# Performance work log

Hardware: AMD Instinct MI355X
Metric: run time of the kernel (lower is better)

The kernel has to match this reference:

```python
import jax, jax.numpy as jnp
import numpy as np

D = 128  # d_pair
N = 512  # n_res
B = 1
EPS = 1e-5


def setup_inputs() -> dict:
    key = jax.random.key(0)
    ks = jax.random.split(key, 16)
    s = 0.02
    inp = {
        "pair": jax.random.normal(ks[0], (B, N, N, D), dtype=jnp.float32),
        "pair_mask": jnp.ones((B, N, N), dtype=jnp.float32),
        "ln_g": jnp.ones((D,), dtype=jnp.float32),
        "ln_b": jnp.zeros((D,), dtype=jnp.float32),
        "w_lp": jax.random.normal(ks[1], (D, D), dtype=jnp.float32) * s,
        "b_lp": jnp.zeros((D,), dtype=jnp.float32),
        "w_lg": jax.random.normal(ks[2], (D, D), dtype=jnp.float32) * s,
        "b_lg": jnp.zeros((D,), dtype=jnp.float32),
        "w_rp": jax.random.normal(ks[3], (D, D), dtype=jnp.float32) * s,
        "b_rp": jnp.zeros((D,), dtype=jnp.float32),
        "w_rg": jax.random.normal(ks[4], (D, D), dtype=jnp.float32) * s,
        "b_rg": jnp.zeros((D,), dtype=jnp.float32),
        "w_g": jax.random.normal(ks[5], (D, D), dtype=jnp.float32) * s,
        "b_g": jnp.zeros((D,), dtype=jnp.float32),
        "w_o": jax.random.normal(ks[6], (D, D), dtype=jnp.float32) * s,
        "b_o": jnp.zeros((D,), dtype=jnp.float32),
    }
    return inp


def _layer_norm(x, g, b):
    mu = jnp.mean(x, axis=-1, keepdims=True)
    var = jnp.mean(jnp.square(x - mu), axis=-1, keepdims=True)
    return (x - mu) * jax.lax.rsqrt(var + EPS) * g + b


def reference(pair, pair_mask, ln_g, ln_b, w_lp, b_lp, w_lg, b_lg,
              w_rp, b_rp, w_rg, b_rg, w_g, b_g, w_o, b_o):
    # [B,N,N,D] pair representation; outgoing triangle multiplication
    x = _layer_norm(pair, ln_g, ln_b)
    mask = pair_mask[..., None]  # [B,N,N,1]
    left = (x @ w_lp + b_lp) * jax.nn.sigmoid(x @ w_lg + b_lg) * mask
    right = (x @ w_rp + b_rp) * jax.nn.sigmoid(x @ w_rg + b_rg) * mask
    # outgoing: contract over j -> per-channel NxN matmul
    out = jnp.einsum('bijd,bjkd->bikd', left, right)
    out = out * jax.nn.sigmoid(x @ w_g + b_g)
    out = out @ w_o + b_o
    return out
```

## Files before the change

kernel.cpp:

```cpp
#include <hip/hip_runtime.h>

#define NN 512
#define DD 128
#define PP (NN*NN)

typedef __attribute__((ext_vector_type(8))) short short8;
typedef __attribute__((ext_vector_type(4))) short shortx4;
typedef __attribute__((ext_vector_type(4))) float floatx4;

__device__ __forceinline__ unsigned short f2bf(float f) {
  unsigned int u = __float_as_uint(f);
  u += 0x7fffu + ((u >> 16) & 1u);
  return (unsigned short)(u >> 16);
}
__device__ __forceinline__ float bf2f(unsigned short h) {
  return __uint_as_float(((unsigned int)h) << 16);
}
__device__ __forceinline__ float sigm(float x) {
  return 1.f / (1.f + __expf(-x));
}

__device__ __forceinline__ void gload_lds16(const unsigned short* g, unsigned short* l) {
  __builtin_amdgcn_global_load_lds(
      (const __attribute__((address_space(1))) unsigned int*)g,
      (__attribute__((address_space(3))) unsigned int*)l, 16, 0, 0);
}

__global__ void k0_prep(const float* __restrict__ wlp, const float* __restrict__ wlg,
                        const float* __restrict__ wrp, const float* __restrict__ wrg,
                        const float* __restrict__ wg,  const float* __restrict__ wo,
                        unsigned short* __restrict__ wt) {
  const float* src[6] = {wlp, wlg, wrp, wrg, wg, wo};
  int m = blockIdx.y;
  int idx = blockIdx.x * 256 + threadIdx.x;
  int d = idx >> 7, e = idx & 127;
  wt[m * 16384 + e * 128 + d] = f2bf(src[m][d * 128 + e]);
}

__device__ __forceinline__ void run_mm(const unsigned short* __restrict__ wt_m,
                                       unsigned short* Alds, unsigned short* Wlds,
                                       int t, int wm, int we, int ln, int q8,
                                       floatx4 (&acc)[4][4]) {
  #pragma unroll
  for (int it = 0; it < 8; ++it) {
    int flat = it * 256 + t;
    int e = flat >> 4, c = flat & 15;
    *(short8*)&Wlds[e * 136 + c * 8] = *(const short8*)(wt_m + e * 128 + c * 8);
  }
  __syncthreads();
  #pragma unroll
  for (int ks = 0; ks < 4; ++ks) {
    short8 a[4], b[4];
    #pragma unroll
    for (int i = 0; i < 4; ++i)
      a[i] = *(const short8*)&Alds[(wm + i * 16 + ln) * 136 + ks * 32 + q8 * 8];
    #pragma unroll
    for (int i = 0; i < 4; ++i)
      b[i] = *(const short8*)&Wlds[(we + i * 16 + ln) * 136 + ks * 32 + q8 * 8];
    #pragma unroll
    for (int i = 0; i < 4; ++i)
      #pragma unroll
      for (int j = 0; j < 4; ++j)
        acc[i][j] = __builtin_amdgcn_mfma_f32_16x16x32_bf16(a[i], b[j], acc[i][j], 0, 0, 0);
  }
  __syncthreads();
}

__launch_bounds__(256, 2)
__global__ void k1_ln_proj(const float* __restrict__ pair, const float* __restrict__ pmask,
                           const float* __restrict__ lng, const float* __restrict__ lnb,
                           const unsigned short* __restrict__ wt,
                           const float* __restrict__ b_lp, const float* __restrict__ b_lg,
                           const float* __restrict__ b_rp, const float* __restrict__ b_rg,
                           const float* __restrict__ b_g,
                           unsigned short* __restrict__ left_t,
                           unsigned short* __restrict__ right_bt,
                           unsigned short* __restrict__ gate_t) {
  __shared__ __align__(16) unsigned short Alds[128 * 136];
  __shared__ __align__(16) unsigned short Wlds[128 * 136];
  __shared__ float Mlds[128];

  const int t = threadIdx.x;
  const int unit = blockIdx.y;
  const int q = blockIdx.x;

  long prow0, pstride, mrow0, mstride, soff;
  if (unit == 1) {
    int j0 = (q >> 9) << 7, k0 = q & 511;
    prow0 = ((long)j0 * NN + k0) * DD; pstride = (long)NN * DD;
    mrow0 = (long)j0 * NN + k0;        mstride = NN;
    soff  = (long)k0 * NN + j0;
  } else {
    long p0 = (long)q << 7;
    prow0 = p0 * DD; pstride = DD;
    mrow0 = p0;      mstride = 1;
    soff  = p0;
  }

  {
    int r = t >> 1, h = t & 1;
    const float* row = pair + prow0 + (long)r * pstride + h * 64;
    floatx4 v[16];
    float s = 0.f, s2 = 0.f;
    #pragma unroll
    for (int c = 0; c < 16; ++c) {
      v[c] = *(const floatx4*)(row + c * 4);
      s  += v[c].x + v[c].y + v[c].z + v[c].w;
      s2 += v[c].x * v[c].x + v[c].y * v[c].y + v[c].z * v[c].z + v[c].w * v[c].w;
    }
    s  += __shfl_xor(s, 1);
    s2 += __shfl_xor(s2, 1);
    float mu = s * (1.f / 128.f);
    float var = s2 * (1.f / 128.f) - mu * mu;
    float rs = rsqrtf(var + 1e-5f);
    #pragma unroll
    for (int c = 0; c < 16; ++c) {
      floatx4 g4 = *(const floatx4*)(lng + h * 64 + c * 4);
      floatx4 b4 = *(const floatx4*)(lnb + h * 64 + c * 4);
      shortx4 pk;
      pk[0] = (short)f2bf((v[c].x - mu) * rs * g4.x + b4.x);
      pk[1] = (short)f2bf((v[c].y - mu) * rs * g4.y + b4.y);
      pk[2] = (short)f2bf((v[c].z - mu) * rs * g4.z + b4.z);
      pk[3] = (short)f2bf((v[c].w - mu) * rs * g4.w + b4.w);
      *(shortx4*)&Alds[r * 136 + h * 64 + c * 4] = pk;
    }
    if (h == 0) Mlds[r] = pmask[mrow0 + (long)r * mstride];
  }
  __syncthreads();

  const int lane = t & 63, w = t >> 6;
  const int ln = lane & 15, q8 = lane >> 4;
  const int wm = (w >> 1) << 6, we = (w & 1) << 6;

  unsigned short* stg = (w < 2) ? (Alds + w * 4608) : (Wlds + (w - 2) * 4608);

  if (unit < 2) {
    floatx4 accA[4][4] = {};
    floatx4 accB[4][4] = {};
    run_mm(wt + (unit == 0 ? 0 : 2) * 16384, Alds, Wlds, t, wm, we, ln, q8, accA);
    run_mm(wt + (unit == 0 ? 1 : 3) * 16384, Alds, Wlds, t, wm, we, ln, q8, accB);
    const float* bpp = (unit == 0) ? b_lp : b_rp;
    const float* bgg = (unit == 0) ? b_lg : b_rg;
    #pragma unroll
    for (int j = 0; j < 4; ++j) {
      int eg = we + j * 16 + ln;
      float bp_v = bpp[eg], bg_v = bgg[eg];
      #pragma unroll
      for (int i = 0; i < 4; ++i) {
        shortx4 pk;
        #pragma unroll
        for (int r = 0; r < 4; ++r) {
          int m = wm + i * 16 + q8 * 4 + r;
          float val = (accA[i][j][r] + bp_v) * sigm(accB[i][j][r] + bg_v) * Mlds[m];
          pk[r] = (short)f2bf(val);
        }
        *(shortx4*)&stg[(j * 16 + ln) * 72 + i * 16 + q8 * 4] = pk;
      }
    }
  } else {
    floatx4 accA[4][4] = {};
    run_mm(wt + 4 * 16384, Alds, Wlds, t, wm, we, ln, q8, accA);
    #pragma unroll
    for (int j = 0; j < 4; ++j) {
      int eg = we + j * 16 + ln;
      float bg_v = b_g[eg];
      #pragma unroll
      for (int i = 0; i < 4; ++i) {
        shortx4 pk;
        #pragma unroll
        for (int r = 0; r < 4; ++r)
          pk[r] = (short)f2bf(sigm(accA[i][j][r] + bg_v));
        *(shortx4*)&stg[(j * 16 + ln) * 72 + i * 16 + q8 * 4] = pk;
      }
    }
  }
  __syncthreads();

  unsigned short* dstbase = (unit == 0) ? left_t : (unit == 1 ? right_bt : gate_t);
  #pragma unroll
  for (int itr = 0; itr < 8; ++itr) {
    int row = itr * 8 + (lane >> 3);
    int c = lane & 7;
    short8 vv = *(const short8*)&stg[row * 72 + c * 8];
    long eg = we + row;
    *(short8*)(dstbase + eg * PP + soff + wm + c * 8) = vv;
  }
}

__launch_bounds__(256, 3)
__global__ void k2_einsum(const unsigned short* __restrict__ left_t,
                          const unsigned short* __restrict__ right_bt,
                          const unsigned short* __restrict__ gate_t,
                          unsigned short* __restrict__ tmpg) {
  __shared__ __align__(16) unsigned short Al[128 * 32];
  __shared__ __align__(16) unsigned short Bl[128 * 32];
  const int t = threadIdx.x;
  const int d = blockIdx.y;
  const int i0 = (blockIdx.x >> 2) << 7;
  const int k0 = (blockIdx.x & 3) << 7;
  const unsigned short* Ag = left_t   + (long)d * PP;
  const unsigned short* Bg = right_bt + (long)d * PP;
  const int lane = t & 63, w = t >> 6;
  const int ln = lane & 15, q8 = lane >> 4;
  const int wm = (w >> 1) << 6, wn = (w & 1) << 6;

  floatx4 acc[4][4] = {};
  for (int j0 = 0; j0 < NN; j0 += 32) {
    #pragma unroll
    for (int it = 0; it < 2; ++it) {
      int flat = it * 256 + t;
      int r = flat >> 2, c = flat & 3;
      gload_lds16(Ag + (long)(i0 + r) * NN + j0 + c * 8, &Al[flat * 8]);
    }
    #pragma unroll
    for (int it = 0; it < 2; ++it) {
      int flat = it * 256 + t;
      int r = flat >> 2, c = flat & 3;
      gload_lds16(Bg + (long)(k0 + r) * NN + j0 + c * 8, &Bl[flat * 8]);
    }
    __syncthreads();
    short8 a[4], b[4];
    #pragma unroll
    for (int i = 0; i < 4; ++i)
      a[i] = *(const short8*)&Al[(wm + i * 16 + ln) * 32 + q8 * 8];
    #pragma unroll
    for (int i = 0; i < 4; ++i)
      b[i] = *(const short8*)&Bl[(wn + i * 16 + ln) * 32 + q8 * 8];
    #pragma unroll
    for (int i = 0; i < 4; ++i)
      #pragma unroll
      for (int j = 0; j < 4; ++j)
        acc[i][j] = __builtin_amdgcn_mfma_f32_16x16x32_bf16(a[i], b[j], acc[i][j], 0, 0, 0);
    __syncthreads();
  }
  const unsigned short* Gg = gate_t + (long)d * PP;
  unsigned short* Og = tmpg + (long)d * PP;
  #pragma unroll
  for (int i = 0; i < 4; ++i)
    #pragma unroll
    for (int j = 0; j < 4; ++j) {
      int n = k0 + wn + j * 16 + ln;
      #pragma unroll
      for (int r = 0; r < 4; ++r) {
        int m = i0 + wm + i * 16 + q8 * 4 + r;
        long idx = (long)m * NN + n;
        Og[idx] = f2bf(acc[i][j][r] * bf2f(Gg[idx]));
      }
    }
}

__launch_bounds__(256, 2)
__global__ void k3_out(const unsigned short* __restrict__ tmpg,
                       const unsigned short* __restrict__ wt,
                       const float* __restrict__ b_o,
                       float* __restrict__ out) {
  __shared__ __align__(16) unsigned short Tl[128 * 136];
  __shared__ __align__(16) unsigned short Wl[128 * 136];
  const int t = threadIdx.x;
  const long p0 = (long)blockIdx.x << 7;
  const unsigned short* wo = wt + 5 * 16384;

  #pragma unroll
  for (int it = 0; it < 8; ++it) {
    int flat = it * 256 + t;
    int e = flat >> 4, c = flat & 15;
    *(short8*)&Wl[e * 136 + c * 8] = *(const short8*)(wo + e * 128 + c * 8);
  }
  #pragma unroll
  for (int it = 0; it < 8; ++it) {
    int flat = it * 256 + t;
    int dd2 = flat >> 4, c = flat & 15;
    *(short8*)&Tl[dd2 * 136 + c * 8] = *(const short8*)(tmpg + (long)dd2 * PP + p0 + c * 8);
  }
  __syncthreads();

  const int lane = t & 63, w = t >> 6;
  const int ln = lane & 15, q8 = lane >> 4;
  const int wm = (w >> 1) << 6, wn = (w & 1) << 6;

  floatx4 acc[4][4] = {};
  #pragma unroll
  for (int ks = 0; ks < 4; ++ks) {
    short8 a[4], b[4];
    #pragma unroll
    for (int i = 0; i < 4; ++i) {
      int m = wm + i * 16 + ln;
      short8 av;
      #pragma unroll
      for (int jj = 0; jj < 8; ++jj)
        av[jj] = (short)Tl[(ks * 32 + q8 * 8 + jj) * 136 + m];
      a[i] = av;
    }
    #pragma unroll
    for (int i = 0; i < 4; ++i)
      b[i] = *(const short8*)&Wl[(wn + i * 16 + ln) * 136 + ks * 32 + q8 * 8];
    #pragma unroll
    for (int i = 0; i < 4; ++i)
      #pragma unroll
      for (int j = 0; j < 4; ++j)
        acc[i][j] = __builtin_amdgcn_mfma_f32_16x16x32_bf16(a[i], b[j], acc[i][j], 0, 0, 0);
  }
  #pragma unroll
  for (int j = 0; j < 4; ++j) {
    int eg = wn + j * 16 + ln;
    float bias = b_o[eg];
    #pragma unroll
    for (int i = 0; i < 4; ++i)
      #pragma unroll
      for (int r = 0; r < 4; ++r) {
        int m = wm + i * 16 + q8 * 4 + r;
        out[(p0 + m) * DD + eg] = acc[i][j][r] + bias;
      }
  }
}

extern "C" void kernel_launch(void* const* d_in, const int* in_sizes, int n_in,
                              void* d_out, int out_size, void* d_ws, size_t ws_size,
                              hipStream_t stream) {
  const float* pair = (const float*)d_in[0];
  const float* pmask = (const float*)d_in[1];
  const float* ln_g = (const float*)d_in[2];
  const float* ln_b = (const float*)d_in[3];
  const float* w_lp = (const float*)d_in[4];
  const float* b_lp = (const float*)d_in[5];
  const float* w_lg = (const float*)d_in[6];
  const float* b_lg = (const float*)d_in[7];
  const float* w_rp = (const float*)d_in[8];
  const float* b_rp = (const float*)d_in[9];
  const float* w_rg = (const float*)d_in[10];
  const float* b_rg = (const float*)d_in[11];
  const float* w_g  = (const float*)d_in[12];
  const float* b_g  = (const float*)d_in[13];
  const float* w_o  = (const float*)d_in[14];
  const float* b_o  = (const float*)d_in[15];
  float* out = (float*)d_out;

  char* ws = (char*)d_ws;
  unsigned short* wt       = (unsigned short*)ws;
  unsigned short* left_t   = (unsigned short*)(ws + 196608);
  unsigned short* right_bt = left_t   + (size_t)PP * DD;
  unsigned short* gate_t   = right_bt + (size_t)PP * DD;
  unsigned short* tmpg     = gate_t   + (size_t)PP * DD;

  k0_prep<<<dim3(64, 6), 256, 0, stream>>>(w_lp, w_lg, w_rp, w_rg, w_g, w_o, wt);
  k1_ln_proj<<<dim3(2048, 3), 256, 0, stream>>>(pair, pmask, ln_g, ln_b, wt,
      b_lp, b_lg, b_rp, b_rg, b_g, left_t, right_bt, gate_t);
  k2_einsum<<<dim3(16, 128), 256, 0, stream>>>(left_t, right_bt, gate_t, tmpg);
  k3_out<<<dim3(2048), 256, 0, stream>>>(tmpg, wt, b_o, out);
}
```

Before: 527.9 us.

## Split layernorm into own kernel, stream projection K-chunks, move gating into output kernel

LayerNorm now runs once in a separate kernel that writes bf16 normalized activations, so the three projection units no longer recompute it from fp32 pair. The projection kernel streams 32-wide K chunks through LDS with direct global-to-LDS loads and fuses the projection and gate matmuls into one loop. The einsum kernel stages its output through LDS so it can write coalesced 16-byte stores without reading the gate. The gate multiply moves into the output kernel, which builds a transposed A tile in LDS and reads W_o straight from global memory. Packed bf16 conversion instructions are also added. The cost is an extra xln buffer round-trip through memory and an extra kernel launch.

```diff
diff --git a/kernel.cpp b/kernel.cpp
--- a/kernel.cpp
+++ b/kernel.cpp
@@ -7,6 +7,7 @@
 typedef __attribute__((ext_vector_type(8))) short short8;
 typedef __attribute__((ext_vector_type(4))) short shortx4;
 typedef __attribute__((ext_vector_type(4))) float floatx4;
+typedef __attribute__((ext_vector_type(4))) unsigned int uintx4;
 
 __device__ __forceinline__ unsigned short f2bf(float f) {
   unsigned int u = __float_as_uint(f);
@@ -15,6 +16,11 @@
 }
 __device__ __forceinline__ float bf2f(unsigned short h) {
   return __uint_as_float(((unsigned int)h) << 16);
+}
+__device__ __forceinline__ unsigned int pkbf2(float lo, float hi) {
+  unsigned int r;
+  asm("v_cvt_pk_bf16_f32 %0, %1, %2" : "=v"(r) : "v"(lo), "v"(hi));
+  return r;
 }
 __device__ __forceinline__ float sigm(float x) {
   return 1.f / (1.f + __expf(-x));
@@ -37,151 +43,166 @@
   wt[m * 16384 + e * 128 + d] = f2bf(src[m][d * 128 + e]);
 }
 
-__device__ __forceinline__ void run_mm(const unsigned short* __restrict__ wt_m,
-                                       unsigned short* Alds, unsigned short* Wlds,
-                                       int t, int wm, int we, int ln, int q8,
-                                       floatx4 (&acc)[4][4]) {
-  #pragma unroll
-  for (int it = 0; it < 8; ++it) {
-    int flat = it * 256 + t;
-    int e = flat >> 4, c = flat & 15;
-    *(short8*)&Wlds[e * 136 + c * 8] = *(const short8*)(wt_m + e * 128 + c * 8);
-  }
-  __syncthreads();
-  #pragma unroll
-  for (int ks = 0; ks < 4; ++ks) {
-    short8 a[4], b[4];
-    #pragma unroll
-    for (int i = 0; i < 4; ++i)
-      a[i] = *(const short8*)&Alds[(wm + i * 16 + ln) * 136 + ks * 32 + q8 * 8];
-    #pragma unroll
-    for (int i = 0; i < 4; ++i)
-      b[i] = *(const short8*)&Wlds[(we + i * 16 + ln) * 136 + ks * 32 + q8 * 8];
-    #pragma unroll
-    for (int i = 0; i < 4; ++i)
-      #pragma unroll
-      for (int j = 0; j < 4; ++j)
-        acc[i][j] = __builtin_amdgcn_mfma_f32_16x16x32_bf16(a[i], b[j], acc[i][j], 0, 0, 0);
-  }
-  __syncthreads();
+__launch_bounds__(256, 4)
+__global__ void k1a_ln(const float* __restrict__ pair,
+                       const float* __restrict__ lng, const float* __restrict__ lnb,
+                       unsigned short* __restrict__ xln) {
+  const int t = threadIdx.x;
+  const long p0 = (long)blockIdx.x << 7;
+  const int r = t >> 1, h = t & 1;
+  const float* row = pair + (p0 + r) * DD + h * 64;
+  floatx4 v[16];
+  float s = 0.f, s2 = 0.f;
+  #pragma unroll
+  for (int c = 0; c < 16; ++c) {
+    v[c] = *(const floatx4*)(row + c * 4);
+    s  += v[c].x + v[c].y + v[c].z + v[c].w;
+    s2 += v[c].x * v[c].x + v[c].y * v[c].y + v[c].z * v[c].z + v[c].w * v[c].w;
+  }
+  s  += __shfl_xor(s, 1);
+  s2 += __shfl_xor(s2, 1);
+  float mu = s * (1.f / 128.f);
+  float var = s2 * (1.f / 128.f) - mu * mu;
+  float rs = rsqrtf(var + 1e-5f);
+  unsigned short* orow = xln + (p0 + r) * DD + h * 64;
+  #pragma unroll
+  for (int c2 = 0; c2 < 8; ++c2) {
+    floatx4 g0 = *(const floatx4*)(lng + h * 64 + c2 * 8);
+    floatx4 g1 = *(const floatx4*)(lng + h * 64 + c2 * 8 + 4);
+    floatx4 b0 = *(const floatx4*)(lnb + h * 64 + c2 * 8);
+    floatx4 b1 = *(const floatx4*)(lnb + h * 64 + c2 * 8 + 4);
+    floatx4 a = v[2 * c2], b = v[2 * c2 + 1];
+    uintx4 u;
+    u[0] = pkbf2((a.x - mu) * rs * g0.x + b0.x, (a.y - mu) * rs * g0.y + b0.y);
+    u[1] = pkbf2((a.z - mu) * rs * g0.z + b0.z, (a.w - mu) * rs * g0.w + b0.w);
+    u[2] = pkbf2((b.x - mu) * rs * g1.x + b1.x, (b.y - mu) * rs * g1.y + b1.y);
+    u[3] = pkbf2((b.z - mu) * rs * g1.z + b1.z, (b.w - mu) * rs * g1.w + b1.w);
+    *(uintx4*)(orow + c2 * 8) = u;
+  }
 }
 
 __launch_bounds__(256, 2)
-__global__ void k1_ln_proj(const float* __restrict__ pair, const float* __restrict__ pmask,
-                           const float* __restrict__ lng, const float* __restrict__ lnb,
-                           const unsigned short* __restrict__ wt,
-                           const float* __restrict__ b_lp, const float* __restrict__ b_lg,
-                           const float* __restrict__ b_rp, const float* __restrict__ b_rg,
-                           const float* __restrict__ b_g,
-                           unsigned short* __restrict__ left_t,
-                           unsigned short* __restrict__ right_bt,
-                           unsigned short* __restrict__ gate_t) {
-  __shared__ __align__(16) unsigned short Alds[128 * 136];
-  __shared__ __align__(16) unsigned short Wlds[128 * 136];
+__global__ void k1b_proj(const unsigned short* __restrict__ xln,
+                         const float* __restrict__ pmask,
+                         const unsigned short* __restrict__ wt,
+                         const float* __restrict__ b_lp, const float* __restrict__ b_lg,
+                         const float* __restrict__ b_rp, const float* __restrict__ b_rg,
+                         const float* __restrict__ b_g,
+                         unsigned short* __restrict__ left_t,
+                         unsigned short* __restrict__ right_bt,
+                         unsigned short* __restrict__ gate_t) {
+  __shared__ __align__(16) unsigned short Sm[17408];
   __shared__ float Mlds[128];
+  unsigned short* Al = Sm;
+  unsigned short* Bp = Sm + 4096;
+  unsigned short* Bg = Sm + 8192;
 
   const int t = threadIdx.x;
   const int unit = blockIdx.y;
   const int q = blockIdx.x;
 
-  long prow0, pstride, mrow0, mstride, soff;
+  int j0 = 0, kk = 0;
+  long p0 = 0, soff;
   if (unit == 1) {
-    int j0 = (q >> 9) << 7, k0 = q & 511;
-    prow0 = ((long)j0 * NN + k0) * DD; pstride = (long)NN * DD;
-    mrow0 = (long)j0 * NN + k0;        mstride = NN;
-    soff  = (long)k0 * NN + j0;
+    j0 = (q >> 9) << 7; kk = q & 511;
+    soff = (long)kk * NN + j0;
   } else {
-    long p0 = (long)q << 7;
-    prow0 = p0 * DD; pstride = DD;
-    mrow0 = p0;      mstride = 1;
-    soff  = p0;
-  }
-
-  {
-    int r = t >> 1, h = t & 1;
-    const float* row = pair + prow0 + (long)r * pstride + h * 64;
-    floatx4 v[16];
-    float s = 0.f, s2 = 0.f;
-    #pragma unroll
-    for (int c = 0; c < 16; ++c) {
-      v[c] = *(const floatx4*)(row + c * 4);
-      s  += v[c].x + v[c].y + v[c].z + v[c].w;
-      s2 += v[c].x * v[c].x + v[c].y * v[c].y + v[c].z * v[c].z + v[c].w * v[c].w;
-    }
-    s  += __shfl_xor(s, 1);
-    s2 += __shfl_xor(s2, 1);
-    float mu = s * (1.f / 128.f);
-    float var = s2 * (1.f / 128.f) - mu * mu;
-    float rs = rsqrtf(var + 1e-5f);
-    #pragma unroll
-    for (int c = 0; c < 16; ++c) {
-      floatx4 g4 = *(const floatx4*)(lng + h * 64 + c * 4);
-      floatx4 b4 = *(const floatx4*)(lnb + h * 64 + c * 4);
-      shortx4 pk;
-      pk[0] = (short)f2bf((v[c].x - mu) * rs * g4.x + b4.x);
-      pk[1] = (short)f2bf((v[c].y - mu) * rs * g4.y + b4.y);
-      pk[2] = (short)f2bf((v[c].z - mu) * rs * g4.z + b4.z);
-      pk[3] = (short)f2bf((v[c].w - mu) * rs * g4.w + b4.w);
-      *(shortx4*)&Alds[r * 136 + h * 64 + c * 4] = pk;
-    }
-    if (h == 0) Mlds[r] = pmask[mrow0 + (long)r * mstride];
-  }
-  __syncthreads();
+    p0 = (long)q << 7;
+    soff = p0;
+  }
+  auto arow = [&](int r) -> long {
+    return (unit == 1) ? ((long)(j0 + r) * NN + kk) : (p0 + r);
+  };
+
+  if (unit < 2 && t < 128) Mlds[t] = pmask[arow(t)];
+
+  const unsigned short* wA = wt + (unit == 0 ? 0 : unit == 1 ? 2 : 4) * 16384;
+  const unsigned short* wB = wt + (unit == 0 ? 1 : 3) * 16384;
 
   const int lane = t & 63, w = t >> 6;
   const int ln = lane & 15, q8 = lane >> 4;
   const int wm = (w >> 1) << 6, we = (w & 1) << 6;
-
-  unsigned short* stg = (w < 2) ? (Alds + w * 4608) : (Wlds + (w - 2) * 4608);
-
+  const int sr = t >> 2, sc = t & 3;
+
+  floatx4 aP[4][4] = {}, aG[4][4] = {};
+  for (int kc = 0; kc < 4; ++kc) {
+    gload_lds16(xln + arow(sr) * DD + kc * 32 + sc * 8,      &Al[t * 8]);
+    gload_lds16(xln + arow(sr + 64) * DD + kc * 32 + sc * 8, &Al[(256 + t) * 8]);
+    gload_lds16(wA + sr * 128 + kc * 32 + sc * 8,            &Bp[t * 8]);
+    gload_lds16(wA + (sr + 64) * 128 + kc * 32 + sc * 8,     &Bp[(256 + t) * 8]);
+    if (unit < 2) {
+      gload_lds16(wB + sr * 128 + kc * 32 + sc * 8,          &Bg[t * 8]);
+      gload_lds16(wB + (sr + 64) * 128 + kc * 32 + sc * 8,   &Bg[(256 + t) * 8]);
+    }
+    __syncthreads();
+    short8 a[4];
+    #pragma unroll
+    for (int i = 0; i < 4; ++i)
+      a[i] = *(const short8*)&Al[(wm + i * 16 + ln) * 32 + q8 * 8];
+    #pragma unroll
+    for (int j = 0; j < 4; ++j) {
+      short8 bpv = *(const short8*)&Bp[(we + j * 16 + ln) * 32 + q8 * 8];
+      #pragma unroll
+      for (int i = 0; i < 4; ++i)
+        aP[i][j] = __builtin_amdgcn_mfma_f32_16x16x32_bf16(a[i], bpv, aP[i][j], 0, 0, 0);
+    }
+    if (unit < 2) {
+      #pragma unroll
+      for (int j = 0; j < 4; ++j) {
+        short8 bgv = *(const short8*)&Bg[(we + j * 16 + ln) * 32 + q8 * 8];
+        #pragma unroll
+        for (int i = 0; i < 4; ++i)
+          aG[i][j] = __builtin_amdgcn_mfma_f32_16x16x32_bf16(a[i], bgv, aG[i][j], 0, 0, 0);
+      }
+    }
+    __syncthreads();
+  }
+
+  unsigned short* mystg = Sm + w * 4352;
   if (unit < 2) {
-    floatx4 accA[4][4] = {};
-    floatx4 accB[4][4] = {};
-    run_mm(wt + (unit == 0 ? 0 : 2) * 16384, Alds, Wlds, t, wm, we, ln, q8, accA);
-    run_mm(wt + (unit == 0 ? 1 : 3) * 16384, Alds, Wlds, t, wm, we, ln, q8, accB);
     const float* bpp = (unit == 0) ? b_lp : b_rp;
     const float* bgg = (unit == 0) ? b_lg : b_rg;
     #pragma unroll
     for (int j = 0; j < 4; ++j) {
       int eg = we + j * 16 + ln;
-      float bp_v = bpp[eg], bg_v = bgg[eg];
+      float bp = bpp[eg], bg = bgg[eg];
       #pragma unroll
       for (int i = 0; i < 4; ++i) {
-        shortx4 pk;
+        float vv[4];
         #pragma unroll
         for (int r = 0; r < 4; ++r) {
           int m = wm + i * 16 + q8 * 4 + r;
-          float val = (accA[i][j][r] + bp_v) * sigm(accB[i][j][r] + bg_v) * Mlds[m];
-          pk[r] = (short)f2bf(val);
+          vv[r] = (aP[i][j][r] + bp) * sigm(aG[i][j][r] + bg) * Mlds[m];
         }
-        *(shortx4*)&stg[(j * 16 + ln) * 72 + i * 16 + q8 * 4] = pk;
+        unsigned int* du = (unsigned int*)&mystg[(j * 16 + ln) * 68 + i * 16 + q8 * 4];
+        du[0] = pkbf2(vv[0], vv[1]);
+        du[1] = pkbf2(vv[2], vv[3]);
       }
     }
   } else {
-    floatx4 accA[4][4] = {};
-    run_mm(wt + 4 * 16384, Alds, Wlds, t, wm, we, ln, q8, accA);
     #pragma unroll
     for (int j = 0; j < 4; ++j) {
       int eg = we + j * 16 + ln;
-      float bg_v = b_g[eg];
+      float bg = b_g[eg];
       #pragma unroll
       for (int i = 0; i < 4; ++i) {
-        shortx4 pk;
+        float vv[4];
         #pragma unroll
         for (int r = 0; r < 4; ++r)
-          pk[r] = (short)f2bf(sigm(accA[i][j][r] + bg_v));
-        *(shortx4*)&stg[(j * 16 + ln) * 72 + i * 16 + q8 * 4] = pk;
+          vv[r] = sigm(aP[i][j][r] + bg);
+        unsigned int* du = (unsigned int*)&mystg[(j * 16 + ln) * 68 + i * 16 + q8 * 4];
+        du[0] = pkbf2(vv[0], vv[1]);
+        du[1] = pkbf2(vv[2], vv[3]);
       }
     }
   }
-  __syncthreads();
 
   unsigned short* dstbase = (unit == 0) ? left_t : (unit == 1 ? right_bt : gate_t);
   #pragma unroll
   for (int itr = 0; itr < 8; ++itr) {
     int row = itr * 8 + (lane >> 3);
     int c = lane & 7;
-    short8 vv = *(const short8*)&stg[row * 72 + c * 8];
+    short8 vv = *(const short8*)&mystg[row * 68 + c * 8];
     long eg = we + row;
     *(short8*)(dstbase + eg * PP + soff + wm + c * 8) = vv;
   }
@@ -190,10 +211,11 @@
 __launch_bounds__(256, 3)
 __global__ void k2_einsum(const unsigned short* __restrict__ left_t,
                           const unsigned short* __restrict__ right_bt,
-                          const unsigned short* __restrict__ gate_t,
                           unsigned short* __restrict__ tmpg) {
-  __shared__ __align__(16) unsigned short Al[128 * 32];
-  __shared__ __align__(16) unsigned short Bl[128 * 32];
+  __shared__ __align__(16) unsigned short Sm[128 * 132];
+  unsigned short* Al = Sm;
+  unsigned short* Bl = Sm + 128 * 32;
+  unsigned short* Cl = Sm;
   const int t = threadIdx.x;
   const int d = blockIdx.y;
   const int i0 = (blockIdx.x >> 2) << 7;
@@ -233,44 +255,58 @@
         acc[i][j] = __builtin_amdgcn_mfma_f32_16x16x32_bf16(a[i], b[j], acc[i][j], 0, 0, 0);
     __syncthreads();
   }
-  const unsigned short* Gg = gate_t + (long)d * PP;
+  #pragma unroll
+  for (int i = 0; i < 4; ++i)
+    #pragma unroll
+    for (int j = 0; j < 4; ++j) {
+      int n = wn + j * 16 + ln;
+      #pragma unroll
+      for (int r = 0; r < 4; ++r)
+        Cl[(wm + i * 16 + q8 * 4 + r) * 132 + n] = f2bf(acc[i][j][r]);
+    }
+  __syncthreads();
   unsigned short* Og = tmpg + (long)d * PP;
   #pragma unroll
-  for (int i = 0; i < 4; ++i)
-    #pragma unroll
-    for (int j = 0; j < 4; ++j) {
-      int n = k0 + wn + j * 16 + ln;
-      #pragma unroll
-      for (int r = 0; r < 4; ++r) {
-        int m = i0 + wm + i * 16 + q8 * 4 + r;
-        long idx = (long)m * NN + n;
-        Og[idx] = f2bf(acc[i][j][r] * bf2f(Gg[idx]));
-      }
-    }
-}
-
-__launch_bounds__(256, 2)
+  for (int it = 0; it < 8; ++it) {
+    int flat = it * 256 + t;
+    int m = flat >> 4, c = flat & 15;
+    *(short8*)(Og + (long)(i0 + m) * NN + k0 + c * 8) = *(const short8*)&Cl[m * 132 + c * 8];
+  }
+}
+
+__launch_bounds__(256, 3)
 __global__ void k3_out(const unsigned short* __restrict__ tmpg,
+                       const unsigned short* __restrict__ gate_t,
                        const unsigned short* __restrict__ wt,
                        const float* __restrict__ b_o,
                        float* __restrict__ out) {
-  __shared__ __align__(16) unsigned short Tl[128 * 136];
-  __shared__ __align__(16) unsigned short Wl[128 * 136];
+  __shared__ __align__(16) unsigned short Tl[128 * 144];
+  unsigned int* TlU = (unsigned int*)Tl;
   const int t = threadIdx.x;
   const long p0 = (long)blockIdx.x << 7;
   const unsigned short* wo = wt + 5 * 16384;
 
   #pragma unroll
-  for (int it = 0; it < 8; ++it) {
+  for (int it = 0; it < 4; ++it) {
     int flat = it * 256 + t;
-    int e = flat >> 4, c = flat & 15;
-    *(short8*)&Wl[e * 136 + c * 8] = *(const short8*)(wo + e * 128 + c * 8);
-  }
-  #pragma unroll
-  for (int it = 0; it < 8; ++it) {
-    int flat = it * 256 + t;
-    int dd2 = flat >> 4, c = flat & 15;
-    *(short8*)&Tl[dd2 * 136 + c * 8] = *(const short8*)(tmpg + (long)dd2 * PP + p0 + c * 8);
+    int rp = flat >> 4;
+    int c  = flat & 15;
+    const unsigned short* ra = tmpg   + (long)(2 * rp) * PP + p0 + c * 8;
+    const unsigned short* ga = gate_t + (long)(2 * rp) * PP + p0 + c * 8;
+    uintx4 xa = *(const uintx4*)ra;
+    uintx4 xb = *(const uintx4*)(ra + PP);
+    uintx4 ya = *(const uintx4*)ga;
+    uintx4 yb = *(const uintx4*)(ga + PP);
+    #pragma unroll
+    for (int cc = 0; cc < 4; ++cc) {
+      float pl = __uint_as_float(xa[cc] << 16) * __uint_as_float(ya[cc] << 16);
+      float ph = __uint_as_float(xa[cc] & 0xffff0000u) * __uint_as_float(ya[cc] & 0xffff0000u);
+      float ql = __uint_as_float(xb[cc] << 16) * __uint_as_float(yb[cc] << 16);
+      float qh = __uint_as_float(xb[cc] & 0xffff0000u) * __uint_as_float(yb[cc] & 0xffff0000u);
+      int p = c * 8 + 2 * cc;
+      TlU[p * 72 + rp]       = pkbf2(pl, ql);
+      TlU[(p + 1) * 72 + rp] = pkbf2(ph, qh);
+    }
   }
   __syncthreads();
 
@@ -283,17 +319,11 @@
   for (int ks = 0; ks < 4; ++ks) {
     short8 a[4], b[4];
     #pragma unroll
-    for (int i = 0; i < 4; ++i) {
-      int m = wm + i * 16 + ln;
-      short8 av;
-      #pragma unroll
-      for (int jj = 0; jj < 8; ++jj)
-        av[jj] = (short)Tl[(ks * 32 + q8 * 8 + jj) * 136 + m];
-      a[i] = av;
-    }
-    #pragma unroll
-    for (int i = 0; i < 4; ++i)
-      b[i] = *(const short8*)&Wl[(wn + i * 16 + ln) * 136 + ks * 32 + q8 * 8];
+    for (int i = 0; i < 4; ++i)
+      a[i] = *(const short8*)&Tl[(wm + i * 16 + ln) * 144 + ks * 32 + q8 * 8];
+    #pragma unroll
+    for (int j = 0; j < 4; ++j)
+      b[j] = *(const short8*)(wo + (wn + j * 16 + ln) * 128 + ks * 32 + q8 * 8);
     #pragma unroll
     for (int i = 0; i < 4; ++i)
       #pragma unroll
@@ -337,14 +367,16 @@
 
   char* ws = (char*)d_ws;
   unsigned short* wt       = (unsigned short*)ws;
-  unsigned short* left_t   = (unsigned short*)(ws + 196608);
+  unsigned short* xln      = (unsigned short*)(ws + 196608);
+  unsigned short* left_t   = xln      + (size_t)PP * DD;
   unsigned short* right_bt = left_t   + (size_t)PP * DD;
   unsigned short* gate_t   = right_bt + (size_t)PP * DD;
-  unsigned short* tmpg     = gate_t   + (size_t)PP * DD;
+  unsigned short* tmpg     = xln;
 
   k0_prep<<<dim3(64, 6), 256, 0, stream>>>(w_lp, w_lg, w_rp, w_rg, w_g, w_o, wt);
-  k1_ln_proj<<<dim3(2048, 3), 256, 0, stream>>>(pair, pmask, ln_g, ln_b, wt,
+  k1a_ln<<<dim3(2048), 256, 0, stream>>>(pair, ln_g, ln_b, xln);
+  k1b_proj<<<dim3(2048, 3), 256, 0, stream>>>(xln, pmask, wt,
       b_lp, b_lg, b_rp, b_rg, b_g, left_t, right_bt, gate_t);
-  k2_einsum<<<dim3(16, 128), 256, 0, stream>>>(left_t, right_bt, gate_t, tmpg);
-  k3_out<<<dim3(2048), 256, 0, stream>>>(tmpg, wt, b_o, out);
-}
+  k2_einsum<<<dim3(16, 128), 256, 0, stream>>>(left_t, right_bt, tmpg);
+  k3_out<<<dim3(2048), 256, 0, stream>>>(tmpg, gate_t, wt, b_o, out);
+}
```

Measured after the change: 516.7 us. 2.1% less time.
